# Performance work log

Hardware: AMD Instinct MI355X
Metric: run time of the kernel (lower is better)

## Reference

```python
import jax, jax.numpy as jnp
import numpy as np

NUM_HEADS = 8
NUM_POINTS = 4


def _bilinear(img, xs, ys):
    """Bilinear sample with zero padding (grid_sample align_corners=False).
    img: [N, H, W, C]; xs, ys: [N, P] pixel-space coords. Returns [N, P, C]."""
    H, W = img.shape[1], img.shape[2]
    x0 = jnp.floor(xs)
    y0 = jnp.floor(ys)
    wx = xs - x0
    wy = ys - y0
    x0i = x0.astype(jnp.int32)
    y0i = y0.astype(jnp.int32)

    def g(ix, iy):
        valid = ((ix >= 0) & (ix < W) & (iy >= 0) & (iy < H)).astype(img.dtype)
        ixc = jnp.clip(ix, 0, W - 1)
        iyc = jnp.clip(iy, 0, H - 1)
        v = jax.vmap(lambda im, yy, xx: im[yy, xx])(img, iyc, ixc)  # [N,P,C]
        return v * valid[..., None]

    return (g(x0i, y0i) * ((1 - wx) * (1 - wy))[..., None]
            + g(x0i + 1, y0i) * (wx * (1 - wy))[..., None]
            + g(x0i, y0i + 1) * ((1 - wx) * wy)[..., None]
            + g(x0i + 1, y0i + 1) * (wx * wy)[..., None])


def setup_inputs() -> dict:
    key = jax.random.key(0)
    ks = jax.random.split(key, 10)
    BN, C, H, W = 12, 256, 40, 100
    nq = H * W
    hp = NUM_HEADS * NUM_POINTS
    s = 1.0 / np.sqrt(C).astype(np.float32)
    return {
        "img_feats": jax.random.normal(ks[0], (BN, C, H, W), jnp.float32),
        "warp_grid": jax.random.uniform(ks[1], (BN, H, W, 2), jnp.float32),
        "reference_points": jax.random.uniform(ks[2], (BN, nq, 1, 2), jnp.float32),
        "Wv": jax.random.normal(ks[3], (C, C), jnp.float32) * s,
        "bv": jnp.zeros((C,), jnp.float32),
        "Woff": jax.random.normal(ks[4], (C, hp * 2), jnp.float32) * 0.01,
        "boff": jax.random.normal(ks[5], (hp * 2,), jnp.float32) * 0.5,
        "Wattn": jax.random.normal(ks[6], (C, hp), jnp.float32) * 0.01,
        "battn": jnp.zeros((hp,), jnp.float32),
        "Wout": jax.random.normal(ks[7], (C, C), jnp.float32) * s,
        "bout": jnp.zeros((C,), jnp.float32),
    }


def reference(img_feats, warp_grid, reference_points,
              Wv, bv, Woff, boff, Wattn, battn, Wout, bout):
    BN, C, H, W = img_feats.shape
    heads, pts = NUM_HEADS, NUM_POINTS
    hd = C // heads
    nq = H * W

    feat = img_feats.transpose(0, 2, 3, 1)  # [BN, H, W, C]

    # BEVWarp: bilinear warp of image features at the projected grid ([0,1] normed)
    gx = warp_grid[..., 0].reshape(BN, -1) * W - 0.5
    gy = warp_grid[..., 1].reshape(BN, -1) * H - 0.5
    warped = _bilinear(feat, gx, gy)          # [BN, nq, C] -> value
    query = feat.reshape(BN, nq, C)           # flattened img feats -> query

    # MultiScaleDeformableAttention, num_levels=1
    v = (warped @ Wv + bv).reshape(BN, nq, heads, hd)
    off = (query @ Woff + boff).reshape(BN, nq, heads, pts, 2)
    attn = jax.nn.softmax((query @ Wattn + battn).reshape(BN, nq, heads, pts), axis=-1)

    norm = jnp.array([W, H], dtype=img_feats.dtype)
    loc = reference_points.reshape(BN, nq, 1, 1, 2) + off / norm  # [BN,nq,h,p,2]

    vh = v.transpose(0, 2, 1, 3).reshape(BN * heads, H, W, hd)
    lx = (loc[..., 0] * W - 0.5).transpose(0, 2, 1, 3).reshape(BN * heads, nq * pts)
    ly = (loc[..., 1] * H - 0.5).transpose(0, 2, 1, 3).reshape(BN * heads, nq * pts)
    sampled = _bilinear(vh, lx, ly).reshape(BN, heads, nq, pts, hd)

    agg = jnp.einsum('bhqpd,bqhp->bqhd', sampled, attn).reshape(BN, nq, C)
    out = agg @ Wout + bout + query  # output_proj + residual (dropout=0 at eval)
    return out.transpose(0, 2, 1).reshape(BN, C, H, W)
```

## Files before the change

kernel.cpp:

```cpp
#include <hip/hip_runtime.h>

#define DEVINL __device__ __forceinline__

typedef __attribute__((ext_vector_type(4))) float f32x4;
typedef __attribute__((ext_vector_type(8))) short short8;

constexpr int kBN = 12, kC = 256, kH = 40, kW = 100;
constexpr int kNQ = kH * kW;
constexpr int kM = kBN * kNQ;

DEVINL float bflo(uint p) { union { uint i; float f; } v; v.i = p << 16; return v.f; }
DEVINL float bfhi(uint p) { union { uint i; float f; } v; v.i = p & 0xffff0000u; return v.f; }
DEVINL ushort f2bf(float f) {
  union { float f; uint i; } v; v.f = f;
  uint i = v.i;
  return (ushort)((i + 0x7fffu + ((i >> 16) & 1u)) >> 16);
}
DEVINL uint pack2(float a, float b) { return (uint)f2bf(a) | ((uint)f2bf(b) << 16); }

DEVINL void mfma_bf16(f32x4& acc, short8 a, short8 b) {
  acc = __builtin_amdgcn_mfma_f32_16x16x32_bf16(a, b, acc, 0, 0, 0);
}

DEVINL void gload16(const ushort* g, char* lds) {
  __builtin_amdgcn_global_load_lds(
      (const __attribute__((address_space(1))) uint*)g,
      (__attribute__((address_space(3))) uint*)lds, 16, 0, 0);
}

DEVINL void acc8(float* acc, uint4 d, float wv) {
  acc[0] += wv * bflo(d.x); acc[1] += wv * bfhi(d.x);
  acc[2] += wv * bflo(d.y); acc[3] += wv * bfhi(d.y);
  acc[4] += wv * bflo(d.z); acc[5] += wv * bfhi(d.z);
  acc[6] += wv * bflo(d.w); acc[7] += wv * bfhi(d.w);
}

__global__ __launch_bounds__(256) void k_wt_all(const float* __restrict__ Wv,
                                                const float* __restrict__ Woff,
                                                const float* __restrict__ Wattn,
                                                const float* __restrict__ Wout,
                                                ushort* __restrict__ WvT,
                                                ushort* __restrict__ WoffT,
                                                ushort* __restrict__ WattnT,
                                                ushort* __restrict__ WoutT) {
  int idx = blockIdx.x * 256 + threadIdx.x;
  const float* W; ushort* WT; int N, base;
  if (idx < 65536)       { W = Wv;    WT = WvT;    N = 256; base = 0; }
  else if (idx < 81920)  { W = Woff;  WT = WoffT;  N = 64;  base = 65536; }
  else if (idx < 90112)  { W = Wattn; WT = WattnT; N = 32;  base = 81920; }
  else if (idx < 155648) { W = Wout;  WT = WoutT;  N = 256; base = 90112; }
  else return;
  int i = idx - base;
  int n = i >> 8, k = i & 255;
  WT[i] = f2bf(W[k * N + n]);
}

__global__ __launch_bounds__(256) void k_transpose(const float* __restrict__ img,
                                                   ushort* __restrict__ feat) {
  __shared__ ushort tile[64][66];
  int b = blockIdx.z, c0 = blockIdx.y * 64, q0 = blockIdx.x * 64;
  int t = threadIdx.x;
  int ql = t & 63, cl = t >> 6;
#pragma unroll
  for (int i = 0; i < 16; ++i) {
    int c = cl + i * 4, q = q0 + ql;
    float v = (q < kNQ) ? img[(size_t)(b * kC + c0 + c) * kNQ + q] : 0.f;
    tile[c][ql] = f2bf(v);
  }
  __syncthreads();
  int cc = t & 63, qr = t >> 6;
#pragma unroll
  for (int i = 0; i < 16; ++i) {
    int qlo = qr + i * 4, q = q0 + qlo;
    if (q < kNQ) feat[(size_t)(b * kNQ + q) * kC + c0 + cc] = tile[cc][qlo];
  }
}

__global__ __launch_bounds__(256) void k_warp(const ushort* __restrict__ feat,
                                              const float* __restrict__ grid,
                                              ushort* __restrict__ warped) {
  int orig = blockIdx.x;
  int n = (orig & 7) * 750 + (orig >> 3);
  int t = threadIdx.x;
  int ql = t >> 5, g = t & 31;
  int gq = n * 8 + ql;
  int b = gq / kNQ;
  float gx = grid[(size_t)gq * 2 + 0] * kW - 0.5f;
  float gy = grid[(size_t)gq * 2 + 1] * kH - 0.5f;
  float x0f = floorf(gx), y0f = floorf(gy);
  int x0 = (int)x0f, y0 = (int)y0f;
  float wx = gx - x0f, wy = gy - y0f;
  float acc[8];
#pragma unroll
  for (int i = 0; i < 8; ++i) acc[i] = 0.f;
  const ushort* fb = feat + (size_t)b * kNQ * kC + g * 8;
#pragma unroll
  for (int ty = 0; ty < 2; ++ty) {
    int iy = y0 + ty;
    if (iy < 0 || iy >= kH) continue;
    float wyv = ty ? wy : 1.f - wy;
#pragma unroll
    for (int tx = 0; tx < 2; ++tx) {
      int ix = x0 + tx;
      if (ix < 0 || ix >= kW) continue;
      float wv = wyv * (tx ? wx : 1.f - wx);
      uint4 d = *(const uint4*)(fb + (size_t)(iy * kW + ix) * kC);
      acc8(acc, d, wv);
    }
  }
  uint o[4] = {pack2(acc[0], acc[1]), pack2(acc[2], acc[3]),
               pack2(acc[4], acc[5]), pack2(acc[6], acc[7])};
  *(uint4*)(warped + (size_t)gq * kC + g * 8) = *(uint4*)o;
}

template <int EPI>
__global__ __launch_bounds__(256) void k_gemm256(const ushort* __restrict__ A,
                                                 const ushort* __restrict__ BT,
                                                 const float* __restrict__ bias,
                                                 ushort* __restrict__ Obf,
                                                 float* __restrict__ Ofp,
                                                 const float* __restrict__ resid) {
  extern __shared__ char smem[];
  const int t = threadIdx.x, wave = t >> 6, lane = t & 63;
  const int l15 = lane & 15, l4 = lane >> 4;
  const int b = blockIdx.x / 63, mb = blockIdx.x % 63;
  const int q0 = mb * 64;
  const int nrows = (kNQ - q0 < 64) ? (kNQ - q0) : 64;
  const int n0w = wave * 64;
  const int ra = t >> 2, ca = t & 3;
  const int sca = ca ^ ((ra >> 1) & 3);
  const ushort* gA = A + ((size_t)b * kNQ + q0 + ra) * 256 + sca * 8;
  const ushort* gB = BT + (size_t)ra * 256 + sca * 8;
  const bool doA = (ra < nrows);

  f32x4 acc[4][4];
#pragma unroll
  for (int i = 0; i < 4; ++i)
#pragma unroll
    for (int j = 0; j < 4; ++j) acc[i][j] = (f32x4)0.f;

  auto STAGE = [&](int buf, int kk) {
    char* Asb = smem + buf * 20480;
    char* Bsb = Asb + 4096;
    if (doA) gload16(gA + kk, Asb + t * 16);
#pragma unroll
    for (int i = 0; i < 4; ++i)
      gload16(gB + (size_t)i * 64 * 256 + kk, Bsb + (i * 256 + t) * 16);
  };

  STAGE(0, 0);
  __syncthreads();
  int cur = 0;
#pragma unroll 1
  for (int step = 0; step < 8; ++step) {
    if (step < 7) STAGE(cur ^ 1, (step + 1) * 32);
    char* Asb = smem + cur * 20480;
    char* Bsb = Asb + 4096;
    short8 af[4], bf[4];
#pragma unroll
    for (int mf = 0; mf < 4; ++mf) {
      int r = mf * 16 + l15;
      int sl = l4 ^ ((r >> 1) & 3);
      af[mf] = *(const short8*)(Asb + r * 64 + sl * 16);
    }
#pragma unroll
    for (int nf = 0; nf < 4; ++nf) {
      int r = n0w + nf * 16 + l15;
      int sl = l4 ^ ((r >> 1) & 3);
      bf[nf] = *(const short8*)(Bsb + r * 64 + sl * 16);
    }
#pragma unroll
    for (int mf = 0; mf < 4; ++mf)
#pragma unroll
      for (int nf = 0; nf < 4; ++nf) mfma_bf16(acc[mf][nf], af[mf], bf[nf]);
    __syncthreads();
    cur ^= 1;
  }

  if (EPI == 0) {
#pragma unroll
    for (int mf = 0; mf < 4; ++mf) {
      if (mf * 16 >= nrows) continue;
      int q = q0 + mf * 16 + l4 * 4;
#pragma unroll
      for (int nf = 0; nf < 4; ++nf) {
        int col = n0w + nf * 16 + l15;
        float bv = bias[col];
        int h = col >> 5, ch = col & 31;
        ushort* dst = Obf + (size_t)(b * 8 + h) * kNQ * 32 + ch;
#pragma unroll
        for (int j = 0; j < 4; ++j)
          dst[(size_t)(q + j) * 32] = f2bf(acc[mf][nf][j] + bv);
      }
    }
  } else {
    float* Tw = (float*)(smem + wave * 4352);
#pragma unroll
    for (int nf = 0; nf < 4; ++nf) {
      float bv = bias[n0w + nf * 16 + l15];
#pragma unroll
      for (int mf = 0; mf < 4; ++mf)
#pragma unroll
        for (int j = 0; j < 4; ++j)
          Tw[l15 * 68 + mf * 16 + l4 * 4 + j] = acc[mf][nf][j] + bv;
      int c = l15, rs = l4 * 16;
      if (rs < nrows) {
        int col = n0w + nf * 16 + c;
        size_t gi = ((size_t)b * kC + col) * kNQ + q0 + rs;
#pragma unroll
        for (int k = 0; k < 4; ++k) {
          float4 tv = *(float4*)(&Tw[c * 68 + rs + k * 4]);
          float4 rv = *(const float4*)(resid + gi + k * 4);
          tv.x += rv.x; tv.y += rv.y; tv.z += rv.z; tv.w += rv.w;
          *(float4*)(Ofp + gi + k * 4) = tv;
        }
      }
    }
  }
}

__global__ __launch_bounds__(256) void k_offattn(const ushort* __restrict__ A,
                                                 const ushort* __restrict__ WoffT,
                                                 const ushort* __restrict__ WattnT,
                                                 const float* __restrict__ boff,
                                                 const float* __restrict__ battn,
                                                 const float* __restrict__ refp,
                                                 float4* __restrict__ samp) {
  extern __shared__ char smem[];
  float* T = (float*)smem;
  const int t = threadIdx.x, wave = t >> 6, lane = t & 63;
  const int l15 = lane & 15, l4 = lane >> 4;
  const int b = blockIdx.x / 63, mb = blockIdx.x % 63;
  const int q0 = mb * 64;
  const int nrows = (kNQ - q0 < 64) ? (kNQ - q0) : 64;
  const int wr = wave >> 1, wc = wave & 1;
  const int ra = t >> 2, ca = t & 3;
  const int sca = ca ^ ((ra >> 1) & 3);
  const ushort* gA  = A + ((size_t)b * kNQ + q0 + ra) * 256 + sca * 8;
  const ushort* gB0 = WoffT + (size_t)ra * 256 + sca * 8;
  const ushort* gB1 = WattnT + (size_t)ra * 256 + sca * 8;
  const bool doA = (ra < nrows);

  f32x4 acc[2][3];
#pragma unroll
  for (int i = 0; i < 2; ++i)
#pragma unroll
    for (int j = 0; j < 3; ++j) acc[i][j] = (f32x4)0.f;

  auto STAGE = [&](int buf, int kk) {
    char* Asb = smem + buf * 10240;
    char* Bsb = Asb + 4096;
    if (doA) gload16(gA + kk, Asb + t * 16);
    gload16(gB0 + kk, Bsb + t * 16);
    if (t < 128) gload16(gB1 + kk, Bsb + (256 + t) * 16);
  };

  STAGE(0, 0);
  __syncthreads();
  int cur = 0;
#pragma unroll 1
  for (int step = 0; step < 8; ++step) {
    if (step < 7) STAGE(cur ^ 1, (step + 1) * 32);
    char* Asb = smem + cur * 10240;
    char* Bsb = Asb + 4096;
    short8 af[2], bf[3];
#pragma unroll
    for (int mf = 0; mf < 2; ++mf) {
      int r = wr * 32 + mf * 16 + l15;
      int sl = l4 ^ ((r >> 1) & 3);
      af[mf] = *(const short8*)(Asb + r * 64 + sl * 16);
    }
#pragma unroll
    for (int nf = 0; nf < 3; ++nf) {
      int r = wc * 48 + nf * 16 + l15;
      int sl = l4 ^ ((r >> 1) & 3);
      bf[nf] = *(const short8*)(Bsb + r * 64 + sl * 16);
    }
#pragma unroll
    for (int mf = 0; mf < 2; ++mf)
#pragma unroll
      for (int nf = 0; nf < 3; ++nf) mfma_bf16(acc[mf][nf], af[mf], bf[nf]);
    __syncthreads();
    cur ^= 1;
  }

#pragma unroll
  for (int nf = 0; nf < 3; ++nf) {
    int col = wc * 48 + nf * 16 + l15;
    float bv = (col < 64) ? boff[col] : battn[col - 64];
#pragma unroll
    for (int mf = 0; mf < 2; ++mf)
#pragma unroll
      for (int j = 0; j < 4; ++j) {
        int row = wr * 32 + mf * 16 + l4 * 4 + j;
        T[row * 101 + col] = acc[mf][nf][j] + bv;
      }
  }
  __syncthreads();
  int row = t >> 2;
  if (row < nrows) {
    int q = q0 + row;
    float refx = refp[((size_t)b * kNQ + q) * 2 + 0] * kW - 0.5f;
    float refy = refp[((size_t)b * kNQ + q) * 2 + 1] * kH - 0.5f;
#pragma unroll
    for (int hi2 = 0; hi2 < 2; ++hi2) {
      int h = (t & 3) + hi2 * 4;
      float sx[4], sy[4], lg[4];
#pragma unroll
      for (int p = 0; p < 4; ++p) {
        sx[p] = refx + T[row * 101 + h * 8 + p * 2 + 0];
        sy[p] = refy + T[row * 101 + h * 8 + p * 2 + 1];
        lg[p] = T[row * 101 + 64 + h * 4 + p];
      }
      float mx = fmaxf(fmaxf(lg[0], lg[1]), fmaxf(lg[2], lg[3]));
      float e[4], s = 0.f;
#pragma unroll
      for (int p = 0; p < 4; ++p) { e[p] = __expf(lg[p] - mx); s += e[p]; }
      float inv = 1.f / s;
      float4* dst = samp + ((size_t)(b * 8 + h) * kNQ + q) * 4;
#pragma unroll
      for (int p = 0; p < 4; ++p) dst[p] = make_float4(sx[p], sy[p], e[p] * inv, 0.f);
    }
  }
}

__global__ __launch_bounds__(256) void k_sample(const ushort* __restrict__ v,
                                                const float4* __restrict__ samp,
                                                ushort* __restrict__ agg) {
  int orig = blockIdx.x;
  int n = (orig & 7) * 756 + (orig >> 3);
  int plane = n / 63, chunk = n - plane * 63;
  int t = threadIdx.x;
  int ql = t >> 2, g = t & 3;
  int q = chunk * 64 + ql;
  if (q >= kNQ) return;
  int b = plane >> 3, h = plane & 7;
  const ushort* pv = v + (size_t)plane * kNQ * 32 + g * 8;
  const int lane = t & 63, gbase = lane & ~3;

  float4 mys = samp[((size_t)plane * kNQ + q) * 4 + g];
  float acc[8];
#pragma unroll
  for (int i = 0; i < 8; ++i) acc[i] = 0.f;
#pragma unroll
  for (int p = 0; p < 4; ++p) {
    float sxp = __shfl(mys.x, gbase + p);
    float syp = __shfl(mys.y, gbase + p);
    float wp  = __shfl(mys.z, gbase + p);
    float x0f = floorf(sxp), y0f = floorf(syp);
    int x0 = (int)x0f, y0 = (int)y0f;
    float wx = sxp - x0f, wy = syp - y0f;
#pragma unroll
    for (int ty = 0; ty < 2; ++ty) {
      int iy = y0 + ty;
      if (iy < 0 || iy >= kH) continue;
      float wyv = ty ? wy : 1.f - wy;
#pragma unroll
      for (int tx = 0; tx < 2; ++tx) {
        int ix = x0 + tx;
        if (ix < 0 || ix >= kW) continue;
        float wv = wp * wyv * (tx ? wx : 1.f - wx);
        uint4 d = *(const uint4*)(pv + (size_t)(iy * kW + ix) * 32);
        acc8(acc, d, wv);
      }
    }
  }
  uint o[4] = {pack2(acc[0], acc[1]), pack2(acc[2], acc[3]),
               pack2(acc[4], acc[5]), pack2(acc[6], acc[7])};
  *(uint4*)(agg + ((size_t)b * kNQ + q) * kC + h * 32 + g * 8) = *(uint4*)o;
}

extern "C" void kernel_launch(void* const* d_in, const int* in_sizes, int n_in,
                              void* d_out, int out_size, void* d_ws, size_t ws_size,
                              hipStream_t stream) {
  const float* img   = (const float*)d_in[0];
  const float* grid  = (const float*)d_in[1];
  const float* refp  = (const float*)d_in[2];
  const float* Wv    = (const float*)d_in[3];
  const float* bv    = (const float*)d_in[4];
  const float* Woff  = (const float*)d_in[5];
  const float* boff  = (const float*)d_in[6];
  const float* Wattn = (const float*)d_in[7];
  const float* battn = (const float*)d_in[8];
  const float* Wout  = (const float*)d_in[9];
  const float* bout  = (const float*)d_in[10];
  float* out = (float*)d_out;

  char* ws = (char*)d_ws;
  const size_t SZ = (size_t)kM * kC * 2;
  ushort* feat   = (ushort*)(ws);
  ushort* warped = (ushort*)(ws + SZ);
  ushort* vbuf   = (ushort*)(ws + 2 * SZ);
  float4* samp   = (float4*)(ws + 3 * SZ);
  ushort* WvT    = (ushort*)(ws + 4 * SZ);
  ushort* WoffT  = (ushort*)(ws + 4 * SZ + 131072);
  ushort* WattnT = (ushort*)(ws + 4 * SZ + 131072 + 32768);
  ushort* WoutT  = (ushort*)(ws + 4 * SZ + 131072 + 32768 + 16384);
  ushort* aggb   = warped;

  k_wt_all<<<608, 256, 0, stream>>>(Wv, Woff, Wattn, Wout, WvT, WoffT, WattnT, WoutT);
  k_transpose<<<dim3(63, 4, 12), 256, 0, stream>>>(img, feat);
  k_warp<<<6000, 256, 0, stream>>>(feat, grid, warped);
  k_gemm256<0><<<756, 256, 40960, stream>>>(warped, WvT, bv, vbuf, nullptr, nullptr);
  k_offattn<<<756, 256, 25856, stream>>>(feat, WoffT, WattnT, boff, battn, refp, samp);
  k_sample<<<6048, 256, 0, stream>>>(vbuf, samp, aggb);
  k_gemm256<1><<<756, 256, 40960, stream>>>(aggb, WoutT, bout, nullptr, out, img);
}
```

Measured before the change: 128.5 us.

## Use explicit vmcnt waits in GEMM pipeline and pack sampling params as float3

The GEMM main loop replaces __syncthreads with raw s_barrier plus explicit s_waitcnt vmcnt, so the next stage's async loads can stay in flight while the current tile is consumed. Out-of-range A rows are clamped to a valid row so every thread issues the same number of loads, which keeps the vmcnt count uniform. Separately, the offset/attention sample buffer drops the padding float, storing 3 floats per point instead of a float4, which cuts write and read traffic between k_offattn and k_sample. The cost is unaligned scalar loads and stores in place of vector ones, and the pipeline now depends on a hand-counted vmcnt value being correct.

```diff
diff --git a/kernel.cpp b/kernel.cpp
--- a/kernel.cpp
+++ b/kernel.cpp
@@ -128,10 +128,10 @@
   const int nrows = (kNQ - q0 < 64) ? (kNQ - q0) : 64;
   const int n0w = wave * 64;
   const int ra = t >> 2, ca = t & 3;
+  const int rac = (ra < nrows) ? ra : (nrows - 1);
   const int sca = ca ^ ((ra >> 1) & 3);
-  const ushort* gA = A + ((size_t)b * kNQ + q0 + ra) * 256 + sca * 8;
+  const ushort* gA = A + ((size_t)b * kNQ + q0 + rac) * 256 + sca * 8;
   const ushort* gB = BT + (size_t)ra * 256 + sca * 8;
-  const bool doA = (ra < nrows);
 
   f32x4 acc[4][4];
 #pragma unroll
@@ -142,18 +142,24 @@
   auto STAGE = [&](int buf, int kk) {
     char* Asb = smem + buf * 20480;
     char* Bsb = Asb + 4096;
-    if (doA) gload16(gA + kk, Asb + t * 16);
+    gload16(gA + kk, Asb + t * 16);
 #pragma unroll
     for (int i = 0; i < 4; ++i)
       gload16(gB + (size_t)i * 64 * 256 + kk, Bsb + (i * 256 + t) * 16);
   };
 
   STAGE(0, 0);
-  __syncthreads();
   int cur = 0;
 #pragma unroll 1
   for (int step = 0; step < 8; ++step) {
-    if (step < 7) STAGE(cur ^ 1, (step + 1) * 32);
+    if (step < 7) {
+      STAGE(cur ^ 1, (step + 1) * 32);
+      asm volatile("s_waitcnt vmcnt(5)" ::: "memory");
+    } else {
+      asm volatile("s_waitcnt vmcnt(0)" ::: "memory");
+    }
+    __builtin_amdgcn_s_barrier();
+    asm volatile("" ::: "memory");
     char* Asb = smem + cur * 20480;
     char* Bsb = Asb + 4096;
     short8 af[4], bf[4];
@@ -173,7 +179,8 @@
     for (int mf = 0; mf < 4; ++mf)
 #pragma unroll
       for (int nf = 0; nf < 4; ++nf) mfma_bf16(acc[mf][nf], af[mf], bf[nf]);
-    __syncthreads();
+    asm volatile("" ::: "memory");
+    __builtin_amdgcn_s_barrier();
     cur ^= 1;
   }
 
@@ -225,7 +232,7 @@
                                                  const float* __restrict__ boff,
                                                  const float* __restrict__ battn,
                                                  const float* __restrict__ refp,
-                                                 float4* __restrict__ samp) {
+                                                 float* __restrict__ samp) {
   extern __shared__ char smem[];
   float* T = (float*)smem;
   const int t = threadIdx.x, wave = t >> 6, lane = t & 63;
@@ -317,15 +324,19 @@
 #pragma unroll
       for (int p = 0; p < 4; ++p) { e[p] = __expf(lg[p] - mx); s += e[p]; }
       float inv = 1.f / s;
-      float4* dst = samp + ((size_t)(b * 8 + h) * kNQ + q) * 4;
-#pragma unroll
-      for (int p = 0; p < 4; ++p) dst[p] = make_float4(sx[p], sy[p], e[p] * inv, 0.f);
+      float* dst = samp + (((size_t)(b * 8 + h) * kNQ + q) * 4) * 3;
+#pragma unroll
+      for (int p = 0; p < 4; ++p) {
+        dst[p * 3 + 0] = sx[p];
+        dst[p * 3 + 1] = sy[p];
+        dst[p * 3 + 2] = e[p] * inv;
+      }
     }
   }
 }
 
 __global__ __launch_bounds__(256) void k_sample(const ushort* __restrict__ v,
-                                                const float4* __restrict__ samp,
+                                                const float* __restrict__ samp,
                                                 ushort* __restrict__ agg) {
   int orig = blockIdx.x;
   int n = (orig & 7) * 756 + (orig >> 3);
@@ -338,15 +349,16 @@
   const ushort* pv = v + (size_t)plane * kNQ * 32 + g * 8;
   const int lane = t & 63, gbase = lane & ~3;
 
-  float4 mys = samp[((size_t)plane * kNQ + q) * 4 + g];
+  const float* sp = samp + (((size_t)plane * kNQ + q) * 4 + g) * 3;
+  float myx = sp[0], myy = sp[1], myw = sp[2];
   float acc[8];
 #pragma unroll
   for (int i = 0; i < 8; ++i) acc[i] = 0.f;
 #pragma unroll
   for (int p = 0; p < 4; ++p) {
-    float sxp = __shfl(mys.x, gbase + p);
-    float syp = __shfl(mys.y, gbase + p);
-    float wp  = __shfl(mys.z, gbase + p);
+    float sxp = __shfl(myx, gbase + p);
+    float syp = __shfl(myy, gbase + p);
+    float wp  = __shfl(myw, gbase + p);
     float x0f = floorf(sxp), y0f = floorf(syp);
     int x0 = (int)x0f, y0 = (int)y0f;
     float wx = sxp - x0f, wy = syp - y0f;
@@ -391,7 +403,7 @@
   ushort* feat   = (ushort*)(ws);
   ushort* warped = (ushort*)(ws + SZ);
   ushort* vbuf   = (ushort*)(ws + 2 * SZ);
-  float4* samp   = (float4*)(ws + 3 * SZ);
+  float*  samp   = (float*)(ws + 3 * SZ);
   ushort* WvT    = (ushort*)(ws + 4 * SZ);
   ushort* WoffT  = (ushort*)(ws + 4 * SZ + 131072);
   ushort* WattnT = (ushort*)(ws + 4 * SZ + 131072 + 32768);
```

New measurement: 123.4 us. 1.04x faster.
